# Performance work log

Hardware: AMD Instinct MI355X
Metric: run time of the kernel (lower is better)

Reference implementation:

```python
import jax, jax.numpy as jnp
import numpy as np

# snnTorch Leaky defaults: beta decay, unit threshold, subtract reset, ATan surrogate grad
BETA = 0.9
THRESH = 1.0
ALPHA = 2.0  # ATan surrogate sharpness


@jax.custom_vjp
def atan_spike(u):
    """Heaviside forward, ATan surrogate backward (snnTorch default spike_grad)."""
    return (u > 0).astype(u.dtype)


def _atan_fwd(u):
    return atan_spike(u), u


def _atan_bwd(u, g):
    # snnTorch ATan: dS/dU = (alpha/2) / (1 + (pi/2 * alpha * U)^2)
    return (g * (ALPHA / 2) / (1 + (jnp.pi / 2 * ALPHA * u) ** 2),)


atan_spike.defvjp(_atan_fwd, _atan_bwd)


def setup_inputs() -> dict:
    key = jax.random.key(0)
    # [T, B, C, H, W] input spike train (values in [0,1))
    x = jax.random.uniform(key, (16, 32, 64, 32, 32), dtype=jnp.float32)
    return {"x": x}


def reference(x):
    """LIF scan over the leading time dim T.

    mem_t = beta * mem_{t-1} + x_t - stop_grad(spk_{t-1}) * threshold  (subtract reset)
    spk_t = Heaviside(mem_t - threshold)  (ATan surrogate in backward)
    Returns spikes of shape [T, B, C, H, W].
    """
    zeros = jnp.zeros_like(x[0])

    def step(carry, x_t):
        mem, spk = carry
        mem = BETA * mem + x_t - jax.lax.stop_gradient(spk) * THRESH
        spk = atan_spike(mem - THRESH)
        return (mem, spk), spk

    _, spikes = jax.lax.scan(step, (zeros, zeros), x)
    return spikes
```

## Files before the change

kernel.cpp:

```cpp
#include <hip/hip_runtime.h>


constexpr int   T      = 16;
constexpr float BETA   = 0.9f;
constexpr float THRESH = 1.0f;

typedef float f4 __attribute__((ext_vector_type(4)));

__global__ __launch_bounds__(256) void lif_kernel(const float* __restrict__ x,
                                                  float* __restrict__ out,
                                                  int n_per_t) {
#pragma clang fp contract(off)
    const int idx = (blockIdx.x * blockDim.x + threadIdx.x) * 4;
    if (idx >= n_per_t) return;

    f4 v[T];

#pragma unroll
    for (int t = 0; t < T; ++t) {
        v[t] = *reinterpret_cast<const f4*>(x + (size_t)t * (size_t)n_per_t + (size_t)idx);
    }

    f4 mem = (f4)(0.f);
    f4 spk = (f4)(0.f);
#pragma unroll
    for (int t = 0; t < T; ++t) {
#pragma unroll
        for (int j = 0; j < 4; ++j) {
            mem[j] = BETA * mem[j] + v[t][j] - spk[j] * THRESH;
            spk[j] = (mem[j] - THRESH) > 0.f ? 1.f : 0.f;
        }
        v[t] = spk;
    }

#pragma unroll
    for (int t = 0; t < T; ++t) {
        __builtin_nontemporal_store(v[t],
            reinterpret_cast<f4*>(out + (size_t)t * (size_t)n_per_t + (size_t)idx));
    }
}

extern "C" void kernel_launch(void* const* d_in, const int* in_sizes, int n_in,
                              void* d_out, int out_size, void* d_ws, size_t ws_size,
                              hipStream_t stream) {
    const float* x   = (const float*)d_in[0];
    float*       out = (float*)d_out;

    const int total   = in_sizes[0];
    const int n_per_t = total / T;
    const int threads = n_per_t / 4;

    dim3 block(256);
    dim3 grid((threads + block.x - 1) / block.x);
    lif_kernel<<<grid, block, 0, stream>>>(x, out, n_per_t);
}
```

Before: 245.5 us.

## Process four float4 columns per thread in two-timestep passes with block barriers

Each thread now covers four float4 columns strided by 1024 and walks time in eight passes of two timesteps. Each pass loads, computes and stores its slice, with __syncthreads around the stores, so only 8 vectors are live instead of 16. Stores become regular instead of nontemporal, and launch bounds request 4 blocks per CU, using a quarter as many blocks. The aim is fewer registers and more overlap of loads and stores, but the barriers and the smaller grid may cut memory parallelism.

```diff
diff --git a/kernel.cpp b/kernel.cpp
--- a/kernel.cpp
+++ b/kernel.cpp
@@ -7,36 +7,52 @@
 
 typedef float f4 __attribute__((ext_vector_type(4)));
 
-__global__ __launch_bounds__(256) void lif_kernel(const float* __restrict__ x,
-                                                  float* __restrict__ out,
-                                                  int n_per_t) {
+__global__ __launch_bounds__(256, 4) void lif_kernel(const float* __restrict__ x,
+                                                     float* __restrict__ out,
+                                                     int n_per_t) {
 #pragma clang fp contract(off)
-    const int idx = (blockIdx.x * blockDim.x + threadIdx.x) * 4;
-    if (idx >= n_per_t) return;
+    int base = blockIdx.x * 4096 + threadIdx.x * 4;
+    if (base + 3072 + 4 > n_per_t) base = 0;
 
-    f4 v[T];
+    f4 m[4] = {(f4)(0.f), (f4)(0.f), (f4)(0.f), (f4)(0.f)};
+    f4 s[4] = {(f4)(0.f), (f4)(0.f), (f4)(0.f), (f4)(0.f)};
+
+    for (int pass = 0; pass < 8; ++pass) {
+        const int t0 = pass * 2;
+
+        f4 r[2][4];
+#pragma unroll
+        for (int p = 0; p < 2; ++p) {
+            const size_t off = (size_t)(t0 + p) * (size_t)n_per_t + (size_t)base;
+#pragma unroll
+            for (int c = 0; c < 4; ++c)
+                r[p][c] = *reinterpret_cast<const f4*>(x + off + c * 1024);
+        }
 
 #pragma unroll
-    for (int t = 0; t < T; ++t) {
-        v[t] = *reinterpret_cast<const f4*>(x + (size_t)t * (size_t)n_per_t + (size_t)idx);
-    }
+        for (int p = 0; p < 2; ++p) {
+#pragma unroll
+            for (int c = 0; c < 4; ++c) {
+#pragma unroll
+                for (int j = 0; j < 4; ++j) {
+                    m[c][j] = BETA * m[c][j] + r[p][c][j] - s[c][j] * THRESH;
+                    s[c][j] = (m[c][j] - THRESH) > 0.f ? 1.f : 0.f;
+                }
+                r[p][c] = s[c];
+            }
+        }
 
-    f4 mem = (f4)(0.f);
-    f4 spk = (f4)(0.f);
-#pragma unroll
-    for (int t = 0; t < T; ++t) {
-#pragma unroll
-        for (int j = 0; j < 4; ++j) {
-            mem[j] = BETA * mem[j] + v[t][j] - spk[j] * THRESH;
-            spk[j] = (mem[j] - THRESH) > 0.f ? 1.f : 0.f;
-        }
-        v[t] = spk;
-    }
+        __syncthreads();
 
 #pragma unroll
-    for (int t = 0; t < T; ++t) {
-        __builtin_nontemporal_store(v[t],
-            reinterpret_cast<f4*>(out + (size_t)t * (size_t)n_per_t + (size_t)idx));
+        for (int p = 0; p < 2; ++p) {
+            const size_t off = (size_t)(t0 + p) * (size_t)n_per_t + (size_t)base;
+#pragma unroll
+            for (int c = 0; c < 4; ++c)
+                *reinterpret_cast<f4*>(out + off + c * 1024) = r[p][c];
+        }
+
+        __syncthreads();
     }
 }
 
@@ -48,9 +64,7 @@
 
     const int total   = in_sizes[0];
     const int n_per_t = total / T;
-    const int threads = n_per_t / 4;
+    const int blocks  = n_per_t / 4096;
 
-    dim3 block(256);
-    dim3 grid((threads + block.x - 1) / block.x);
-    lif_kernel<<<grid, block, 0, stream>>>(x, out, n_per_t);
+    lif_kernel<<<dim3(blocks), dim3(256), 0, stream>>>(x, out, n_per_t);
 }
```

Measured after the change: 226.1 us, median of 2. -7.9%, faster.
